# Kernel optimization log

Hardware: AMD Instinct MI355X
Metric: run time of the kernel (lower is better)

The kernel has to match this reference:

```python
import jax, jax.numpy as jnp
import numpy as np
from jax import lax

AGG_HOPS = 3
RANK_K = 10
NEG = -1e9


def _aggregate(embs, agg_w, agg_b, W_last, b_last):
    # GIKT-style multi-hop mean aggregation: embs[j] has shape [B, n1..nj, D]
    embs = list(embs)
    for i in range(AGG_HOPS):
        for j in range(AGG_HOPS - i):
            s = jnp.mean(embs[j + 1], axis=-2) + embs[j]
            embs[j] = jnp.tanh(s @ agg_w[j].T + agg_b[j])
    return jnp.tanh(embs[0] @ W_last.T + b_last)


def _hops(nodes0, tabA, tabB):
    # alternating bipartite neighbor expansion: [B] -> [B,n] -> [B,n,n] -> ...
    lst = [nodes0]
    for i in range(AGG_HOPS):
        tab = tabA if i % 2 == 0 else tabB
        lst.append(tab[lst[-1]])
    return lst


def _forward(user, question, response, mask, q_neighbors, s_neighbors, u_neighbors,
             q_neighbors_2, qs_index, emb_question, emb_question_2, emb_skill,
             emb_user, emb_response, w1_q, w2_q, W_ih, W_hh, b_ih, b_hh,
             agg_w, agg_b, W_agg_last, b_agg_last, W_query, b_query, W_key, b_key,
             W_w, b_w, W_fusion, b_fusion):
    B, T = question.shape
    D = emb_question.shape[1]
    emb_q_all = emb_question[question]  # [B,T,D], used for recap similarity
    wA, wB = W_w[0, :D], W_w[0, D:]     # MLP_W(cat(Q,K)) = Q@wA + K@wB + b

    def predict(qs_concat, states, svalid):
        ql = (qs_concat @ W_query.T + b_query) @ wA          # [B,Lq]
        kl = (states @ W_key.T + b_key) @ wB                 # [B,Ls]
        logit = ql[:, :, None] + kl[:, None, :] + b_w[0]     # [B,Lq,Ls]
        logit = jnp.where(svalid[:, None, :], logit, NEG)
        Lq, Ls = logit.shape[1], logit.shape[2]
        alpha = jax.nn.softmax(logit.reshape(B, -1), axis=1).reshape(B, Lq, Ls)
        g = jnp.einsum('bqd,bsd->bqs', qs_concat, states)
        return jax.nn.sigmoid(jnp.sum(alpha * g, axis=(1, 2)))

    def step(carry, t):
        h, c, sh = carry
        q_t, u_t, r_t = question[:, t], user[:, t], response[:, t]
        m = (mask[:, t] == 1)[:, None]  # [B,1]
        # question-skill GNN branch
        embs_q = [(emb_question if i % 2 == 0 else emb_skill)[n]
                  for i, n in enumerate(_hops(q_t, q_neighbors, s_neighbors))]
        e1 = jnp.where(m, _aggregate(embs_q, agg_w, agg_b, W_agg_last, b_agg_last),
                       emb_question[q_t])
        # user-question GNN branch
        embs_u = [(emb_user if i % 2 == 0 else emb_question_2)[n]
                  for i, n in enumerate(_hops(u_t, u_neighbors, q_neighbors_2))]
        e2 = jnp.where(m, _aggregate(embs_u, agg_w, agg_b, W_agg_last, b_agg_last),
                       emb_question_2[q_t])
        e_hat = w1_q * e1 + w2_q * e2
        e_t = jax.nn.relu(jnp.concatenate([e_hat, emb_response[r_t]], axis=1)
                          @ W_fusion.T + b_fusion)
        # masked LSTMCell (torch gate order i,f,g,o); dropout in eval mode
        gates = e_t @ W_ih.T + b_ih + h @ W_hh.T + b_hh
        gi, gf, gg, go = jnp.split(gates, 4, axis=1)
        c2 = jax.nn.sigmoid(gf) * c + jax.nn.sigmoid(gi) * jnp.tanh(gg)
        h2 = jax.nn.sigmoid(go) * jnp.tanh(c2)
        h = jnp.where(m, h2, h)
        c = jnp.where(m, c2, c)
        sh = lax.dynamic_update_slice(sh, h[:, None, :], (0, t, 0))
        # next question + its related skills
        q_next = question[:, t + 1]
        emb_qn = emb_question[q_next]
        qs_concat = jnp.concatenate([emb_qn[:, None, :], emb_skill[qs_index[q_next]]], axis=1)
        # soft recap: top-k past states by (detached) question similarity
        scores = lax.stop_gradient(jnp.einsum('btd,bd->bt', emb_q_all, emb_qn))
        valid_t = jnp.arange(T) < t
        scores = jnp.where(valid_t[None, :], scores, NEG)
        _, idx = lax.top_k(scores, RANK_K)                    # [B,K]
        sel = jnp.take_along_axis(sh, idx[:, :, None], axis=1)  # [B,K,D]
        svalid = jnp.concatenate([jnp.ones((B, 1), bool), valid_t[idx]], axis=1)
        states = jnp.concatenate([h[:, None, :], sel], axis=1)  # [B,1+K,D]
        y = predict(qs_concat, states, svalid)
        return (h, c, sh), y

    h0 = jnp.zeros((B, D), jnp.float32)
    sh0 = jnp.zeros((B, T, D), jnp.float32)
    _, ys = lax.scan(step, (h0, h0, sh0), jnp.arange(T - 1))
    return jnp.concatenate([jnp.full((B, 1), 0.5, jnp.float32), ys.T], axis=1)


def setup_inputs() -> dict:
    B, T, D = 32, 50, 100
    NQ, NS, NU = 20000, 500, 10000
    NBR, SPQ = 6, 4
    key = jax.random.key(0)
    ks = iter(jax.random.split(key, 48))
    nrm = lambda shape, sc: jax.random.normal(next(ks), shape, jnp.float32) * sc
    ri = lambda shape, hi: jax.random.randint(next(ks), shape, 0, hi, jnp.int32)
    s = 1.0 / float(np.sqrt(D))
    return {
        'user': ri((B, T), NU), 'question': ri((B, T), NQ),
        'response': ri((B, T), 2), 'mask': ri((B, T), 2),
        'q_neighbors': ri((NQ, NBR), NS), 's_neighbors': ri((NS, NBR), NQ),
        'u_neighbors': ri((NU, NBR), NQ), 'q_neighbors_2': ri((NQ, NBR), NU),
        'qs_index': ri((NQ, SPQ), NS),
        'emb_question': nrm((NQ, D), 0.1), 'emb_question_2': nrm((NQ, D), 0.1),
        'emb_skill': nrm((NS, D), 0.1), 'emb_user': nrm((NU, D), 0.1),
        'emb_response': nrm((2, D), 0.1),
        'w1_q': jnp.float32(0.5), 'w2_q': jnp.float32(0.5),
        'W_ih': nrm((4 * D, D), s), 'W_hh': nrm((4 * D, D), s),
        'b_ih': jnp.zeros((4 * D,), jnp.float32), 'b_hh': jnp.zeros((4 * D,), jnp.float32),
        'agg_w': nrm((3, D, D), s), 'agg_b': jnp.zeros((3, D), jnp.float32),
        'W_agg_last': nrm((D, D), s), 'b_agg_last': jnp.zeros((D,), jnp.float32),
        'W_query': nrm((D, D), s), 'b_query': jnp.zeros((D,), jnp.float32),
        'W_key': nrm((D, D), s), 'b_key': jnp.zeros((D,), jnp.float32),
        'W_w': nrm((1, 2 * D), s), 'b_w': jnp.zeros((1,), jnp.float32),
        'W_fusion': nrm((D, 2 * D), s), 'b_fusion': jnp.zeros((D,), jnp.float32),
    }


def reference(user, question, response, mask, q_neighbors, s_neighbors, u_neighbors,
              q_neighbors_2, qs_index, emb_question, emb_question_2, emb_skill,
              emb_user, emb_response, w1_q, w2_q, W_ih, W_hh, b_ih, b_hh,
              agg_w, agg_b, W_agg_last, b_agg_last, W_query, b_query, W_key, b_key,
              W_w, b_w, W_fusion, b_fusion):
    return _forward(user, question, response, mask, q_neighbors, s_neighbors,
                    u_neighbors, q_neighbors_2, qs_index, emb_question,
                    emb_question_2, emb_skill, emb_user, emb_response, w1_q, w2_q,
                    W_ih, W_hh, b_ih, b_hh, agg_w, agg_b, W_agg_last, b_agg_last,
                    W_query, b_query, W_key, b_key, W_w, b_w, W_fusion, b_fusion)
```

## Files before the change

### kernel.cpp

```cpp
#include <hip/hip_runtime.h>
#include <hip/hip_bf16.h>

#define BSZ 32
#define TT 50
#define TS 49
#define PH 101

#define OFF_GPRE  0u
#define OFF_QL    627200u
#define OFF_IDX   639744u
#define OFF_NV    655424u
#define OFF_QSC   656992u
#define OFF_E1    1440992u
#define OFF_E2    1597792u

#define RLF(v,l) __uint_as_float(__builtin_amdgcn_readlane(__float_as_uint(v), (l)))

__device__ __forceinline__ float tanh_fast(float x) {
    float e = __expf(2.f * x);
    return 1.f - __fdividef(2.f, e + 1.f);
}
__device__ __forceinline__ float sigm_fast(float x) {
    return __fdividef(1.f, 1.f + __expf(-x));
}
__device__ __forceinline__ float dot4(float4 a, float4 b) {
    return a.x*b.x + a.y*b.y + a.z*b.z + a.w*b.w;
}
__device__ __forceinline__ float dot100(const float* __restrict__ w, const float* __restrict__ x) {
    float acc = 0.f;
    for (int k = 0; k < 100; k += 4)
        acc += dot4(*(const float4*)(w + k), *(const float4*)(x + k));
    return acc;
}

__global__ __launch_bounds__(384, 5) void kagg(
    const int* __restrict__ user, const int* __restrict__ question, const int* __restrict__ mask,
    const int* __restrict__ qnbr, const int* __restrict__ snbr,
    const int* __restrict__ unbr, const int* __restrict__ qnbr2,
    const float* __restrict__ embQ, const float* __restrict__ embQ2, const float* __restrict__ embS,
    const float* __restrict__ embU,
    const float* __restrict__ aggw, const float* __restrict__ aggb,
    const float* __restrict__ wlast, const float* __restrict__ blast,
    float* __restrict__ WS)
{
    int bid = blockIdx.x;
    int pair = bid >> 1, which = bid & 1;
    int b = pair / TS, t = pair - b*TS;
    int tid = threadIdx.x;
    int mm = mask[b*TT + t];
    float* outE = WS + (which ? OFF_E2 : OFF_E1) + (size_t)pair*100;

    if (mm != 1) {
        int q_t = question[b*TT + t];
        const float* src = which ? embQ2 : embQ;
        if (tid < 100) outE[tid] = src[(size_t)q_t*100 + tid];
        return;
    }

    int root = which ? user[b*TT + t] : question[b*TT + t];
    const int*   tabA = which ? unbr  : qnbr;
    const int*   tabB = which ? qnbr2 : snbr;
    const float* embE = which ? embU  : embQ;
    const float* embO = which ? embQ2 : embS;

    __shared__ __align__(16) float b2in[36*108];
    __shared__ __align__(16) float x1[6*108];
    __shared__ float s2v1b[600];
    __shared__ float v1a[600];
    __shared__ __align__(16) float x0[104], v0a[104], v0b[104];
    __shared__ int n1[8], n2[36], n3[216];

    if (tid < 6) n1[tid] = tabA[root*6 + tid];
    __syncthreads();
    if (tid < 36) n2[tid] = tabB[n1[tid/6]*6 + (tid % 6)];
    __syncthreads();
    if (tid < 216) n3[tid] = tabA[n2[tid/6]*6 + (tid % 6)];
    __syncthreads();
    for (int e = tid; e < 3600; e += 384) {
        int v = e / 100, d = e - v*100;
        float acc = embE[(size_t)n2[v]*100 + d];
        float s3 = 0.f;
        const int* p = n3 + v*6;
        for (int c = 0; c < 6; ++c) s3 += embO[(size_t)p[c]*100 + d];
        b2in[v*108 + d] = acc + s3 * (1.f/6.f);
    }
    for (int e = tid; e < 600; e += 384) {
        int a = e / 100, d = e - a*100;
        float acc = embO[(size_t)n1[a]*100 + d];
        float s = 0.f;
        for (int c = 0; c < 6; ++c) s += embE[(size_t)n2[a*6 + c]*100 + d];
        x1[a*108 + d] = acc + s * (1.f/6.f);
    }
    if (tid < 100) {
        float acc = embE[(size_t)root*100 + tid];
        float s = 0.f;
        for (int a = 0; a < 6; ++a) s += embO[(size_t)n1[a]*100 + tid];
        x0[tid] = acc + s * (1.f/6.f);
    }
    __syncthreads();
    if (tid < 300) {
        int dblk = tid / 6, a = tid - dblk*6, d0 = dblk*2;
        const float* wp = aggw + 20000 + d0*100;
        const float* xb = b2in + a*648;
        float a0[6], a1[6];
        #pragma unroll
        for (int c = 0; c < 6; ++c) { a0[c] = 0.f; a1[c] = 0.f; }
        #pragma unroll
        for (int j = 0; j < 25; ++j) {
            float4 r0 = *(const float4*)(wp + 4*j);
            float4 r1 = *(const float4*)(wp + 100 + 4*j);
            #pragma unroll
            for (int c = 0; c < 6; ++c) {
                float4 x = *(const float4*)(xb + c*108 + 4*j);
                a0[c] += dot4(r0, x);
                a1[c] += dot4(r1, x);
            }
        }
        float bi0 = aggb[200 + d0], bi1 = aggb[200 + d0 + 1];
        float o0 = 0.f, o1 = 0.f;
        #pragma unroll
        for (int c = 0; c < 6; ++c) { o0 += tanh_fast(bi0 + a0[c]); o1 += tanh_fast(bi1 + a1[c]); }
        s2v1b[a*100 + d0] = o0; s2v1b[a*100 + d0 + 1] = o1;
    } else if (tid < 350) {
        int d0 = (tid - 300)*2;
        const float* wp = aggw + 10000 + d0*100;
        float a0[6], a1[6];
        #pragma unroll
        for (int c = 0; c < 6; ++c) { a0[c] = 0.f; a1[c] = 0.f; }
        #pragma unroll
        for (int j = 0; j < 25; ++j) {
            float4 r0 = *(const float4*)(wp + 4*j);
            float4 r1 = *(const float4*)(wp + 100 + 4*j);
            #pragma unroll
            for (int c = 0; c < 6; ++c) {
                float4 x = *(const float4*)(x1 + c*108 + 4*j);
                a0[c] += dot4(r0, x);
                a1[c] += dot4(r1, x);
            }
        }
        #pragma unroll
        for (int c = 0; c < 6; ++c) {
            v1a[c*100 + d0]     = tanh_fast(aggb[100 + d0] + a0[c]);
            v1a[c*100 + d0 + 1] = tanh_fast(aggb[100 + d0 + 1] + a1[c]);
        }
    } else if (tid < 375) {
        int d0 = (tid - 350)*4;
        const float* wp = aggw + d0*100;
        float a0 = 0.f, a1 = 0.f, a2 = 0.f, a3 = 0.f;
        #pragma unroll
        for (int j = 0; j < 25; ++j) {
            float4 x = *(const float4*)(x0 + 4*j);
            a0 += dot4(*(const float4*)(wp + 4*j), x);
            a1 += dot4(*(const float4*)(wp + 100 + 4*j), x);
            a2 += dot4(*(const float4*)(wp + 200 + 4*j), x);
            a3 += dot4(*(const float4*)(wp + 300 + 4*j), x);
        }
        v0a[d0]   = tanh_fast(aggb[d0] + a0);
        v0a[d0+1] = tanh_fast(aggb[d0+1] + a1);
        v0a[d0+2] = tanh_fast(aggb[d0+2] + a2);
        v0a[d0+3] = tanh_fast(aggb[d0+3] + a3);
    }
    __syncthreads();
    for (int e = tid; e < 600; e += 384) {
        int a = e / 100, d = e - a*100;
        x1[a*108 + d] = v1a[a*100 + d] + s2v1b[a*100 + d]*(1.f/6.f);
    }
    if (tid < 100) {
        float s = 0.f;
        for (int a = 0; a < 6; ++a) s += v1a[a*100 + tid];
        x0[tid] = v0a[tid] + s*(1.f/6.f);
    }
    __syncthreads();
    if (tid < 50) {
        int d0 = tid*2;
        const float* wp = aggw + 10000 + d0*100;
        float a0[6], a1[6];
        #pragma unroll
        for (int c = 0; c < 6; ++c) { a0[c] = 0.f; a1[c] = 0.f; }
        #pragma unroll
        for (int j = 0; j < 25; ++j) {
            float4 r0 = *(const float4*)(wp + 4*j);
            float4 r1 = *(const float4*)(wp + 100 + 4*j);
            #pragma unroll
            for (int c = 0; c < 6; ++c) {
                float4 x = *(const float4*)(x1 + c*108 + 4*j);
                a0[c] += dot4(r0, x);
                a1[c] += dot4(r1, x);
            }
        }
        #pragma unroll
        for (int c = 0; c < 6; ++c) {
            s2v1b[c*100 + d0]     = tanh_fast(aggb[100 + d0] + a0[c]);
            s2v1b[c*100 + d0 + 1] = tanh_fast(aggb[100 + d0 + 1] + a1[c]);
        }
    } else if (tid >= 64 && tid < 89) {
        int d0 = (tid - 64)*4;
        const float* wp = aggw + d0*100;
        float a0 = 0.f, a1 = 0.f, a2 = 0.f, a3 = 0.f;
        #pragma unroll
        for (int j = 0; j < 25; ++j) {
            float4 x = *(const float4*)(x0 + 4*j);
            a0 += dot4(*(const float4*)(wp + 4*j), x);
            a1 += dot4(*(const float4*)(wp + 100 + 4*j), x);
            a2 += dot4(*(const float4*)(wp + 200 + 4*j), x);
            a3 += dot4(*(const float4*)(wp + 300 + 4*j), x);
        }
        v0b[d0]   = tanh_fast(aggb[d0] + a0);
        v0b[d0+1] = tanh_fast(aggb[d0+1] + a1);
        v0b[d0+2] = tanh_fast(aggb[d0+2] + a2);
        v0b[d0+3] = tanh_fast(aggb[d0+3] + a3);
    }
    __syncthreads();
    if (tid < 100) {
        float s = 0.f;
        for (int a = 0; a < 6; ++a) s += s2v1b[a*100 + tid];
        x0[tid] = v0b[tid] + s*(1.f/6.f);
    }
    __syncthreads();
    if (tid < 25) {
        int d0 = tid*4;
        const float* wp = aggw + d0*100;
        float a0 = 0.f, a1 = 0.f, a2 = 0.f, a3 = 0.f;
        #pragma unroll
        for (int j = 0; j < 25; ++j) {
            float4 x = *(const float4*)(x0 + 4*j);
            a0 += dot4(*(const float4*)(wp + 4*j), x);
            a1 += dot4(*(const float4*)(wp + 100 + 4*j), x);
            a2 += dot4(*(const float4*)(wp + 200 + 4*j), x);
            a3 += dot4(*(const float4*)(wp + 300 + 4*j), x);
        }
        v0a[d0]   = tanh_fast(aggb[d0] + a0);
        v0a[d0+1] = tanh_fast(aggb[d0+1] + a1);
        v0a[d0+2] = tanh_fast(aggb[d0+2] + a2);
        v0a[d0+3] = tanh_fast(aggb[d0+3] + a3);
    }
    __syncthreads();
    if (tid < 25) {
        int d0 = tid*4;
        const float* wp = wlast + d0*100;
        float a0 = 0.f, a1 = 0.f, a2 = 0.f, a3 = 0.f;
        #pragma unroll
        for (int j = 0; j < 25; ++j) {
            float4 x = *(const float4*)(v0a + 4*j);
            a0 += dot4(*(const float4*)(wp + 4*j), x);
            a1 += dot4(*(const float4*)(wp + 100 + 4*j), x);
            a2 += dot4(*(const float4*)(wp + 200 + 4*j), x);
            a3 += dot4(*(const float4*)(wp + 300 + 4*j), x);
        }
        outE[d0]   = tanh_fast(blast[d0] + a0);
        outE[d0+1] = tanh_fast(blast[d0+1] + a1);
        outE[d0+2] = tanh_fast(blast[d0+2] + a2);
        outE[d0+3] = tanh_fast(blast[d0+3] + a3);
    }
}

__global__ __launch_bounds__(256) void kfuse(
    const int* __restrict__ question, const int* __restrict__ response,
    const int* __restrict__ qsidx,
    const float* __restrict__ embQ, const float* __restrict__ embS, const float* __restrict__ embR,
    const float* __restrict__ w1p, const float* __restrict__ w2p,
    const float* __restrict__ wfus, const float* __restrict__ bfus,
    const float* __restrict__ wih, const float* __restrict__ bih, const float* __restrict__ bhh,
    const float* __restrict__ wq, const float* __restrict__ bq, const float* __restrict__ ww,
    float* __restrict__ WS)
{
    int bid = blockIdx.x;
    int b = bid / TS, t = bid - b*TS;
    int tid = threadIdx.x;
    size_t bt = (size_t)b*TS + t;

    __shared__ __align__(16) float sEIN[200], sET[104], sEQN[104], sVQ[104];
    __shared__ float sWW[200], sQSCm[500], sScore[56], sCq[1];

    int r_t = response[b*TT + t];
    int qn  = question[b*TT + t + 1];
    float w1 = w1p[0], w2 = w2p[0];
    if (tid < 100)
        sEIN[tid] = w1*WS[OFF_E1 + bt*100 + tid] + w2*WS[OFF_E2 + bt*100 + tid];
    else if (tid < 200)
        sEIN[tid] = embR[r_t*100 + (tid - 100)];
    else
        for (int i = tid - 200; i < 200; i += 56) sWW[i] = ww[i];
    __syncthreads();
    if (tid < 100) {
        float acc = bfus[tid];
        const float* wr = wfus + tid*200;
        for (int k = 0; k < 200; k += 4)
            acc += dot4(*(const float4*)(wr + k), *(const float4*)(sEIN + k));
        sET[tid] = fmaxf(acc, 0.f);
    } else if (tid < 200) {
        int k = tid - 100;
        float acc = 0.f;
        for (int d = 0; d < 100; ++d) acc += sWW[d]*wq[d*100 + k];
        sVQ[k] = acc;
    } else if (tid == 200) {
        float acc = 0.f;
        for (int d = 0; d < 100; ++d) acc += bq[d]*sWW[d];
        sCq[0] = acc;
    } else if (tid >= 201 && tid < 251) {
        int d = tid - 201;
        sEQN[d]      = embQ[(size_t)qn*100 + d];
        sEQN[d + 50] = embQ[(size_t)qn*100 + d + 50];
    }
    __syncthreads();
    if (tid < 200) {
        for (int i = tid; i < 500; i += 200) {
            int q = i / 100, d = i - q*100;
            float val = (q == 0) ? sEQN[d] : embS[(size_t)qsidx[qn*4 + (q-1)]*100 + d];
            sQSCm[i] = val;
            WS[OFF_QSC + bt*500 + i] = val;
        }
    } else if (tid < 250) {
        int tp = tid - 200;
        if (tp < t) {
            int qq = question[b*TT + tp];
            const float* er = embQ + (size_t)qq*100;
            float acc = 0.f;
            for (int k = 0; k < 100; k += 4)
                acc += dot4(*(const float4*)(er + k), *(const float4*)(sEQN + k));
            sScore[tp] = acc;
        }
    }
    __syncthreads();
    for (int o = tid; o < 400; o += 256)
        WS[OFF_GPRE + bt*400 + o] = bih[o] + bhh[o] + dot100(wih + o*100, sET);
    if (tid < 80) {
        int q = tid >> 4, k0 = tid & 15;
        float acc = 0.f;
        #pragma unroll
        for (int j = 0; j < 7; ++j) {
            int k = k0 + 16*j;
            if (k < 100) acc = fmaf(sQSCm[q*100 + k], sVQ[k], acc);
        }
        acc += __shfl_xor(acc, 1); acc += __shfl_xor(acc, 2);
        acc += __shfl_xor(acc, 4); acc += __shfl_xor(acc, 8);
        if (k0 == 0) WS[OFF_QL + bt*8 + q] = acc + sCq[0];
    }
    if (tid == 255) {
        int nv = t < 10 ? t : 10;
        ((int*)(WS + OFF_NV))[bt] = nv;
        int* idxp = (int*)(WS + OFF_IDX) + bt*10;
        unsigned long long taken = 0ull;
        for (int p = 0; p < 10; ++p) {
            int bi = 0;
            if (p < nv) {
                float best = -3.0e38f;
                for (int tp2 = 0; tp2 < t; ++tp2) {
                    if (!((taken >> tp2) & 1ull) && sScore[tp2] > best) { best = sScore[tp2]; bi = tp2; }
                }
                taken |= (1ull << bi);
            }
            idxp[p] = bi;
        }
    }
}

__global__ __launch_bounds__(576) void kseq(
    const int* __restrict__ mask, const float* __restrict__ whh,
    const float* __restrict__ wk, const float* __restrict__ bk,
    const float* __restrict__ ww, const float* __restrict__ bwp,
    const float* __restrict__ WS, float* __restrict__ out)
{
    int b = blockIdx.x, tid = threadIdx.x, lane = tid & 63;
    __shared__ float sQSCall[TS*500];
    __shared__ float sSH[TS*PH + 3];
    __shared__ float sQLall[TS*8];
    __shared__ int   sIdxAll[TS*10];
    __shared__ int   sNvAll[TS];
    __shared__ int   sMask[TT];
    __shared__ float sH[104], sC[104], sG[400], sVKl[104];
    __shared__ float sKL2[2][12], sGv2[2][64];
    __shared__ float sCkBw[2];

    size_t b0 = (size_t)b*TS;
    int g = tid - 64;
    bool isGate = (g >= 0 && g < 400);

    float4 wv[25];
    if (isGate) {
        #pragma unroll
        for (int j = 0; j < 25; ++j) wv[j] = *(const float4*)(whh + g*100 + 4*j);
    }
    float gpre = isGate ? WS[OFF_GPRE + b0*400 + g] : 0.f;

    for (int i = tid; i < TS*500; i += 576) sQSCall[i] = WS[OFF_QSC + b0*500 + i];
    for (int i = tid; i < TS*8;   i += 576) sQLall[i]  = WS[OFF_QL + b0*8 + i];
    for (int i = tid; i < TS*10;  i += 576) sIdxAll[i] = ((const int*)(WS + OFF_IDX))[b0*10 + i];
    for (int i = tid; i < TS;     i += 576) sNvAll[i]  = ((const int*)(WS + OFF_NV))[b0 + i];
    if (tid < TT) sMask[tid] = mask[b*TT + tid];
    if (tid < 104) { sH[tid] = 0.f; sC[tid] = 0.f; }
    if (tid >= 104 && tid < 204) {
        int k = tid - 104;
        float acc = 0.f;
        for (int d = 0; d < 100; ++d) acc += ww[100 + d]*wk[d*100 + k];
        sVKl[k] = acc;
    }
    if (tid == 204) {
        float acc = 0.f;
        for (int d = 0; d < 100; ++d) acc += bk[d]*ww[100 + d];
        sCkBw[0] = acc; sCkBw[1] = bwp[0];
    }
    if (tid == 205) out[b*TT] = 0.5f;
    __syncthreads();
    float ck = sCkBw[0], bw = sCkBw[1];

    for (int t = 0; t < TS; ++t) {
        int par = t & 1;
        if (isGate) {
            float hA = sH[lane];
            float hB = sH[64 + (lane % 36)];
            float gpre_nx = 0.f;
            if (t + 1 < TS) gpre_nx = WS[OFF_GPRE + (b0 + t + 1)*400 + g];
            float a0 = 0.f, a1 = 0.f, a2 = 0.f, a3 = 0.f;
            #pragma unroll
            for (int j = 0; j < 25; ++j) {
                const int kb = 4*j;
                float h0, h1, h2, h3;
                if (kb < 64) {
                    h0 = RLF(hA, kb);   h1 = RLF(hA, kb+1);
                    h2 = RLF(hA, kb+2); h3 = RLF(hA, kb+3);
                } else {
                    h0 = RLF(hB, kb-64); h1 = RLF(hB, kb-63);
                    h2 = RLF(hB, kb-62); h3 = RLF(hB, kb-61);
                }
                a0 = fmaf(h0, wv[j].x, a0);
                a1 = fmaf(h1, wv[j].y, a1);
                a2 = fmaf(h2, wv[j].z, a2);
                a3 = fmaf(h3, wv[j].w, a3);
            }
            sG[g] = (a0 + a1) + (a2 + a3) + gpre;
            gpre = gpre_nx;
        } else if (tid >= 512) {
            int nv = sNvAll[t];
            if (lane < 60) {
                bool isKL = lane < 10;
                int s = isKL ? (lane + 1) : (((lane - 10) % 10) + 1);
                int q = isKL ? 0 : ((lane - 10) / 10);
                if (s <= nv) {
                    const float* st = sSH + sIdxAll[t*10 + s - 1]*PH;
                    const float* xp = isKL ? sVKl : (sQSCall + t*500 + q*100);
                    float c0 = 0.f, c1 = 0.f, c2 = 0.f, c3 = 0.f;
                    #pragma unroll
                    for (int k = 0; k < 100; k += 4) {
                        c0 = fmaf(st[k],   xp[k],   c0);
                        c1 = fmaf(st[k+1], xp[k+1], c1);
                        c2 = fmaf(st[k+2], xp[k+2], c2);
                        c3 = fmaf(st[k+3], xp[k+3], c3);
                    }
                    float acc = (c0 + c1) + (c2 + c3);
                    if (isKL) sKL2[par][s] = acc + ck;
                    else      sGv2[par][q*12 + s] = acc;
                }
            }
        } else if (tid < 64 && t > 0) {
            int tau = t - 1, par2 = tau & 1;
            int nv = sNvAll[tau];
            int dd = lane >> 3, k0 = lane & 7;
            if (dd < 6) {
                const float* xp = (dd == 0) ? sVKl : (sQSCall + tau*500 + (dd-1)*100);
                float acc = 0.f;
                #pragma unroll
                for (int jj = 0; jj < 13; ++jj) {
                    int k = k0 + 8*jj;
                    if (k < 100) acc = fmaf(sH[k], xp[k], acc);
                }
                acc += __shfl_xor(acc, 1); acc += __shfl_xor(acc, 2); acc += __shfl_xor(acc, 4);
                if (k0 == 0) {
                    if (dd == 0) sKL2[par2][0] = acc + ck;
                    else         sGv2[par2][(dd-1)*12] = acc;
                }
            }
            int q = lane / 11, s = lane - q*11;
            bool valid = (lane < 55) && (s <= nv);
            float lg = valid ? (sQLall[tau*8 + q] + sKL2[par2][s] + bw) : 0.f;
            float e  = valid ? __expf(lg) : 0.f;
            float gv = valid ? sGv2[par2][q*12 + s] : 0.f;
            float se = e, sg = e*gv;
            #pragma unroll
            for (int m = 1; m < 64; m <<= 1) { se += __shfl_xor(se, m); sg += __shfl_xor(sg, m); }
            if (lane == 0) out[b*TT + tau + 1] = __fdividef(1.f, 1.f + __expf(-__fdividef(sg, se)));
        }
        __syncthreads();
        if (g >= 0 && g < 100) {
            float gi = sG[g], gf = sG[100+g], gg = sG[200+g], go = sG[300+g];
            float c2 = sigm_fast(gf)*sC[g] + sigm_fast(gi)*tanh_fast(gg);
            float h2 = sigm_fast(go)*tanh_fast(c2);
            if (sMask[t] == 1) { sH[g] = h2; sC[g] = c2; }
            sSH[t*PH + g] = sH[g];
        }
        __syncthreads();
    }
    if (tid < 64) {
        int tau = TS - 1, par2 = tau & 1;
        int nv = sNvAll[tau];
        int dd = lane >> 3, k0 = lane & 7;
        if (dd < 6) {
            const float* xp = (dd == 0) ? sVKl : (sQSCall + tau*500 + (dd-1)*100);
            float acc = 0.f;
            #pragma unroll
            for (int jj = 0; jj < 13; ++jj) {
                int k = k0 + 8*jj;
                if (k < 100) acc = fmaf(sH[k], xp[k], acc);
            }
            acc += __shfl_xor(acc, 1); acc += __shfl_xor(acc, 2); acc += __shfl_xor(acc, 4);
            if (k0 == 0) {
                if (dd == 0) sKL2[par2][0] = acc + ck;
                else         sGv2[par2][(dd-1)*12] = acc;
            }
        }
        int q = lane / 11, s = lane - q*11;
        bool valid = (lane < 55) && (s <= nv);
        float lg = valid ? (sQLall[tau*8 + q] + sKL2[par2][s] + bw) : 0.f;
        float e  = valid ? __expf(lg) : 0.f;
        float gv = valid ? sGv2[par2][q*12 + s] : 0.f;
        float se = e, sg = e*gv;
        #pragma unroll
        for (int m = 1; m < 64; m <<= 1) { se += __shfl_xor(se, m); sg += __shfl_xor(sg, m); }
        if (lane == 0) out[b*TT + tau + 1] = __fdividef(1.f, 1.f + __expf(-__fdividef(sg, se)));
    }
}

extern "C" void kernel_launch(void* const* d_in, const int* in_sizes, int n_in,
                              void* d_out, int out_size, void* d_ws, size_t ws_size,
                              hipStream_t stream) {
    const int* user      = (const int*)d_in[0];
    const int* question  = (const int*)d_in[1];
    const int* response  = (const int*)d_in[2];
    const int* mask      = (const int*)d_in[3];
    const int* qnbr      = (const int*)d_in[4];
    const int* snbr      = (const int*)d_in[5];
    const int* unbr      = (const int*)d_in[6];
    const int* qnbr2     = (const int*)d_in[7];
    const int* qsidx     = (const int*)d_in[8];
    const float* embQ    = (const float*)d_in[9];
    const float* embQ2   = (const float*)d_in[10];
    const float* embS    = (const float*)d_in[11];
    const float* embU    = (const float*)d_in[12];
    const float* embR    = (const float*)d_in[13];
    const float* w1      = (const float*)d_in[14];
    const float* w2      = (const float*)d_in[15];
    const float* wih     = (const float*)d_in[16];
    const float* whh     = (const float*)d_in[17];
    const float* bih     = (const float*)d_in[18];
    const float* bhh     = (const float*)d_in[19];
    const float* aggw    = (const float*)d_in[20];
    const float* aggb    = (const float*)d_in[21];
    const float* wlast   = (const float*)d_in[22];
    const float* blast   = (const float*)d_in[23];
    const float* wq      = (const float*)d_in[24];
    const float* bq      = (const float*)d_in[25];
    const float* wk      = (const float*)d_in[26];
    const float* bk      = (const float*)d_in[27];
    const float* ww      = (const float*)d_in[28];
    const float* bwp     = (const float*)d_in[29];
    const float* wfus    = (const float*)d_in[30];
    const float* bfus    = (const float*)d_in[31];
    float* WS = (float*)d_ws;
    float* out = (float*)d_out;

    hipLaunchKernelGGL(kagg, dim3(2*BSZ*TS), dim3(384), 0, stream,
                       user, question, mask, qnbr, snbr, unbr, qnbr2,
                       embQ, embQ2, embS, embU, aggw, aggb, wlast, blast, WS);
    hipLaunchKernelGGL(kfuse, dim3(BSZ*TS), dim3(256), 0, stream,
                       question, response, qsidx, embQ, embS, embR,
                       w1, w2, wfus, bfus, wih, bih, bhh, wq, bq, ww, WS);
    hipLaunchKernelGGL(kseq, dim3(BSZ), dim3(576), 0, stream,
                       mask, whh, wk, bk, ww, bwp, WS, out);
}
```

Baseline: 438.4 us.

## Hoist weight-vector precompute, vectorize gathers, parallelize fuse matvecs and top-k

The constant query/key projection vectors (W_w folded into W_query/W_key and their biases) are now computed once by an extra block in the aggregation kernel, instead of once per (b,t) block in kfuse and once per batch in kseq. The aggregation kernel shrinks to 256 threads, uses float4 gathers of the embedding rows and gives each thread 4 output rows in the hop-2 matvec. kfuse now computes its fusion and gate-input matvecs with 16-lane cooperative dot products and shuffle reductions. Its serial single-thread top-10 selection becomes a wave-wide argmax reduction. These changes add a cross-kernel dependency on the workspace constants and rely on the extra block finishing before kfuse reads them.

```diff
diff --git a/kernel.cpp b/kernel.cpp
--- a/kernel.cpp
+++ b/kernel.cpp
@@ -6,13 +6,16 @@
 #define TS 49
 #define PH 101
 
-#define OFF_GPRE  0u
-#define OFF_QL    627200u
-#define OFF_IDX   639744u
-#define OFF_NV    655424u
-#define OFF_QSC   656992u
-#define OFF_E1    1440992u
-#define OFF_E2    1597792u
+#define OFF_VQ    0u
+#define OFF_VK    128u
+#define OFF_SC    256u
+#define OFF_GPRE  288u
+#define OFF_QL    627488u
+#define OFF_IDX   640032u
+#define OFF_NV    655712u
+#define OFF_QSC   657280u
+#define OFF_E1    1441280u
+#define OFF_E2    1598080u
 
 #define RLF(v,l) __uint_as_float(__builtin_amdgcn_readlane(__float_as_uint(v), (l)))
 
@@ -26,14 +29,8 @@
 __device__ __forceinline__ float dot4(float4 a, float4 b) {
     return a.x*b.x + a.y*b.y + a.z*b.z + a.w*b.w;
 }
-__device__ __forceinline__ float dot100(const float* __restrict__ w, const float* __restrict__ x) {
-    float acc = 0.f;
-    for (int k = 0; k < 100; k += 4)
-        acc += dot4(*(const float4*)(w + k), *(const float4*)(x + k));
-    return acc;
-}
-
-__global__ __launch_bounds__(384, 5) void kagg(
+
+__global__ __launch_bounds__(256, 5) void kagg(
     const int* __restrict__ user, const int* __restrict__ question, const int* __restrict__ mask,
     const int* __restrict__ qnbr, const int* __restrict__ snbr,
     const int* __restrict__ unbr, const int* __restrict__ qnbr2,
@@ -41,19 +38,47 @@
     const float* __restrict__ embU,
     const float* __restrict__ aggw, const float* __restrict__ aggb,
     const float* __restrict__ wlast, const float* __restrict__ blast,
+    const float* __restrict__ wq, const float* __restrict__ bq,
+    const float* __restrict__ wk, const float* __restrict__ bk,
+    const float* __restrict__ ww, const float* __restrict__ bwp,
     float* __restrict__ WS)
 {
     int bid = blockIdx.x;
+    int tid = threadIdx.x;
+
+    if (bid == 2*BSZ*TS) {
+        if (tid < 100) {
+            float a = 0.f;
+            for (int d = 0; d < 100; ++d) a += ww[d] * wq[d*100 + tid];
+            WS[OFF_VQ + tid] = a;
+        } else if (tid < 200) {
+            int k = tid - 100;
+            float a = 0.f;
+            for (int d = 0; d < 100; ++d) a += ww[100 + d] * wk[d*100 + k];
+            WS[OFF_VK + k] = a;
+        } else if (tid == 200) {
+            float a = 0.f;
+            for (int d = 0; d < 100; ++d) a += bq[d] * ww[d];
+            WS[OFF_SC + 0] = a;
+        } else if (tid == 201) {
+            float a = 0.f;
+            for (int d = 0; d < 100; ++d) a += bk[d] * ww[100 + d];
+            WS[OFF_SC + 1] = a;
+        } else if (tid == 202) {
+            WS[OFF_SC + 2] = bwp[0];
+        }
+        return;
+    }
+
     int pair = bid >> 1, which = bid & 1;
     int b = pair / TS, t = pair - b*TS;
-    int tid = threadIdx.x;
     int mm = mask[b*TT + t];
     float* outE = WS + (which ? OFF_E2 : OFF_E1) + (size_t)pair*100;
 
     if (mm != 1) {
         int q_t = question[b*TT + t];
-        const float* src = which ? embQ2 : embQ;
-        if (tid < 100) outE[tid] = src[(size_t)q_t*100 + tid];
+        const float4* src = (const float4*)((which ? embQ2 : embQ) + (size_t)q_t*100);
+        if (tid < 25) ((float4*)outE)[tid] = src[tid];
         return;
     }
 
@@ -62,6 +87,8 @@
     const int*   tabB = which ? qnbr2 : snbr;
     const float* embE = which ? embU  : embQ;
     const float* embO = which ? embQ2 : embS;
+    const float4* eE = (const float4*)embE;
+    const float4* eO = (const float4*)embO;
 
     __shared__ __align__(16) float b2in[36*108];
     __shared__ __align__(16) float x1[6*108];
@@ -76,53 +103,81 @@
     __syncthreads();
     if (tid < 216) n3[tid] = tabA[n2[tid/6]*6 + (tid % 6)];
     __syncthreads();
-    for (int e = tid; e < 3600; e += 384) {
-        int v = e / 100, d = e - v*100;
-        float acc = embE[(size_t)n2[v]*100 + d];
-        float s3 = 0.f;
+    for (int i4 = tid; i4 < 900; i4 += 256) {
+        int v = i4 / 25, j = i4 - v*25;
+        float4 a = eE[(size_t)n2[v]*25 + j];
+        float4 s = make_float4(0.f, 0.f, 0.f, 0.f);
         const int* p = n3 + v*6;
-        for (int c = 0; c < 6; ++c) s3 += embO[(size_t)p[c]*100 + d];
-        b2in[v*108 + d] = acc + s3 * (1.f/6.f);
-    }
-    for (int e = tid; e < 600; e += 384) {
-        int a = e / 100, d = e - a*100;
-        float acc = embO[(size_t)n1[a]*100 + d];
-        float s = 0.f;
-        for (int c = 0; c < 6; ++c) s += embE[(size_t)n2[a*6 + c]*100 + d];
-        x1[a*108 + d] = acc + s * (1.f/6.f);
-    }
-    if (tid < 100) {
-        float acc = embE[(size_t)root*100 + tid];
-        float s = 0.f;
-        for (int a = 0; a < 6; ++a) s += embO[(size_t)n1[a]*100 + tid];
-        x0[tid] = acc + s * (1.f/6.f);
-    }
-    __syncthreads();
-    if (tid < 300) {
-        int dblk = tid / 6, a = tid - dblk*6, d0 = dblk*2;
+        #pragma unroll
+        for (int c = 0; c < 6; ++c) {
+            float4 o = eO[(size_t)p[c]*25 + j];
+            s.x += o.x; s.y += o.y; s.z += o.z; s.w += o.w;
+        }
+        float4 r = make_float4(a.x + s.x*(1.f/6.f), a.y + s.y*(1.f/6.f),
+                               a.z + s.z*(1.f/6.f), a.w + s.w*(1.f/6.f));
+        *(float4*)(b2in + v*108 + 4*j) = r;
+    }
+    for (int i4 = tid; i4 < 150; i4 += 256) {
+        int a = i4 / 25, j = i4 - a*25;
+        float4 base = eO[(size_t)n1[a]*25 + j];
+        float4 s = make_float4(0.f, 0.f, 0.f, 0.f);
+        #pragma unroll
+        for (int c = 0; c < 6; ++c) {
+            float4 o = eE[(size_t)n2[a*6 + c]*25 + j];
+            s.x += o.x; s.y += o.y; s.z += o.z; s.w += o.w;
+        }
+        float4 r = make_float4(base.x + s.x*(1.f/6.f), base.y + s.y*(1.f/6.f),
+                               base.z + s.z*(1.f/6.f), base.w + s.w*(1.f/6.f));
+        *(float4*)(x1 + a*108 + 4*j) = r;
+    }
+    if (tid >= 160 && tid < 185) {
+        int j = tid - 160;
+        float4 base = eE[(size_t)root*25 + j];
+        float4 s = make_float4(0.f, 0.f, 0.f, 0.f);
+        #pragma unroll
+        for (int a = 0; a < 6; ++a) {
+            float4 o = eO[(size_t)n1[a]*25 + j];
+            s.x += o.x; s.y += o.y; s.z += o.z; s.w += o.w;
+        }
+        float4 r = make_float4(base.x + s.x*(1.f/6.f), base.y + s.y*(1.f/6.f),
+                               base.z + s.z*(1.f/6.f), base.w + s.w*(1.f/6.f));
+        *(float4*)(x0 + 4*j) = r;
+    }
+    __syncthreads();
+    if (tid < 150) {
+        int dblk = tid / 6, a = tid - dblk*6, d0 = dblk*4;
         const float* wp = aggw + 20000 + d0*100;
         const float* xb = b2in + a*648;
-        float a0[6], a1[6];
-        #pragma unroll
-        for (int c = 0; c < 6; ++c) { a0[c] = 0.f; a1[c] = 0.f; }
+        float acc[4][6];
+        #pragma unroll
+        for (int r = 0; r < 4; ++r)
+            #pragma unroll
+            for (int c = 0; c < 6; ++c) acc[r][c] = 0.f;
         #pragma unroll
         for (int j = 0; j < 25; ++j) {
             float4 r0 = *(const float4*)(wp + 4*j);
             float4 r1 = *(const float4*)(wp + 100 + 4*j);
+            float4 r2 = *(const float4*)(wp + 200 + 4*j);
+            float4 r3 = *(const float4*)(wp + 300 + 4*j);
             #pragma unroll
             for (int c = 0; c < 6; ++c) {
                 float4 x = *(const float4*)(xb + c*108 + 4*j);
-                a0[c] += dot4(r0, x);
-                a1[c] += dot4(r1, x);
-            }
-        }
-        float bi0 = aggb[200 + d0], bi1 = aggb[200 + d0 + 1];
-        float o0 = 0.f, o1 = 0.f;
-        #pragma unroll
-        for (int c = 0; c < 6; ++c) { o0 += tanh_fast(bi0 + a0[c]); o1 += tanh_fast(bi1 + a1[c]); }
-        s2v1b[a*100 + d0] = o0; s2v1b[a*100 + d0 + 1] = o1;
-    } else if (tid < 350) {
-        int d0 = (tid - 300)*2;
+                acc[0][c] += dot4(r0, x);
+                acc[1][c] += dot4(r1, x);
+                acc[2][c] += dot4(r2, x);
+                acc[3][c] += dot4(r3, x);
+            }
+        }
+        #pragma unroll
+        for (int r = 0; r < 4; ++r) {
+            float bia = aggb[200 + d0 + r];
+            float o = 0.f;
+            #pragma unroll
+            for (int c = 0; c < 6; ++c) o += tanh_fast(bia + acc[r][c]);
+            s2v1b[a*100 + d0 + r] = o;
+        }
+    } else if (tid >= 160 && tid < 210) {
+        int d0 = (tid - 160)*2;
         const float* wp = aggw + 10000 + d0*100;
         float a0[6], a1[6];
         #pragma unroll
@@ -143,8 +198,8 @@
             v1a[c*100 + d0]     = tanh_fast(aggb[100 + d0] + a0[c]);
             v1a[c*100 + d0 + 1] = tanh_fast(aggb[100 + d0 + 1] + a1[c]);
         }
-    } else if (tid < 375) {
-        int d0 = (tid - 350)*4;
+    } else if (tid >= 216 && tid < 241) {
+        int d0 = (tid - 216)*4;
         const float* wp = aggw + d0*100;
         float a0 = 0.f, a1 = 0.f, a2 = 0.f, a3 = 0.f;
         #pragma unroll
@@ -161,14 +216,16 @@
         v0a[d0+3] = tanh_fast(aggb[d0+3] + a3);
     }
     __syncthreads();
-    for (int e = tid; e < 600; e += 384) {
+    for (int e = tid; e < 600; e += 256) {
         int a = e / 100, d = e - a*100;
         x1[a*108 + d] = v1a[a*100 + d] + s2v1b[a*100 + d]*(1.f/6.f);
     }
-    if (tid < 100) {
+    if (tid >= 128 && tid < 228) {
+        int d = tid - 128;
         float s = 0.f;
-        for (int a = 0; a < 6; ++a) s += v1a[a*100 + tid];
-        x0[tid] = v0a[tid] + s*(1.f/6.f);
+        #pragma unroll
+        for (int a = 0; a < 6; ++a) s += v1a[a*100 + d];
+        x0[d] = v0a[d] + s*(1.f/6.f);
     }
     __syncthreads();
     if (tid < 50) {
@@ -213,6 +270,7 @@
     __syncthreads();
     if (tid < 100) {
         float s = 0.f;
+        #pragma unroll
         for (int a = 0; a < 6; ++a) s += s2v1b[a*100 + tid];
         x0[tid] = v0b[tid] + s*(1.f/6.f);
     }
@@ -247,21 +305,19 @@
             a2 += dot4(*(const float4*)(wp + 200 + 4*j), x);
             a3 += dot4(*(const float4*)(wp + 300 + 4*j), x);
         }
-        outE[d0]   = tanh_fast(blast[d0] + a0);
-        outE[d0+1] = tanh_fast(blast[d0+1] + a1);
-        outE[d0+2] = tanh_fast(blast[d0+2] + a2);
-        outE[d0+3] = tanh_fast(blast[d0+3] + a3);
+        float4 r = make_float4(tanh_fast(blast[d0] + a0), tanh_fast(blast[d0+1] + a1),
+                               tanh_fast(blast[d0+2] + a2), tanh_fast(blast[d0+3] + a3));
+        *(float4*)(outE + d0) = r;
     }
 }
 
-__global__ __launch_bounds__(256) void kfuse(
+__global__ __launch_bounds__(256, 6) void kfuse(
     const int* __restrict__ question, const int* __restrict__ response,
     const int* __restrict__ qsidx,
     const float* __restrict__ embQ, const float* __restrict__ embS, const float* __restrict__ embR,
     const float* __restrict__ w1p, const float* __restrict__ w2p,
     const float* __restrict__ wfus, const float* __restrict__ bfus,
     const float* __restrict__ wih, const float* __restrict__ bih, const float* __restrict__ bhh,
-    const float* __restrict__ wq, const float* __restrict__ bq, const float* __restrict__ ww,
     float* __restrict__ WS)
 {
     int bid = blockIdx.x;
@@ -269,96 +325,113 @@
     int tid = threadIdx.x;
     size_t bt = (size_t)b*TS + t;
 
-    __shared__ __align__(16) float sEIN[200], sET[104], sEQN[104], sVQ[104];
-    __shared__ float sWW[200], sQSCm[500], sScore[56], sCq[1];
+    __shared__ __align__(16) float sEIN[200], sET[112], sEQN[104], sQSCm[500];
+    __shared__ float sScore[52];
 
     int r_t = response[b*TT + t];
     int qn  = question[b*TT + t + 1];
-    float w1 = w1p[0], w2 = w2p[0];
-    if (tid < 100)
-        sEIN[tid] = w1*WS[OFF_E1 + bt*100 + tid] + w2*WS[OFF_E2 + bt*100 + tid];
-    else if (tid < 200)
+    if (tid < 100) {
+        sEIN[tid] = w1p[0]*WS[OFF_E1 + bt*100 + tid] + w2p[0]*WS[OFF_E2 + bt*100 + tid];
+    } else if (tid < 200) {
         sEIN[tid] = embR[r_t*100 + (tid - 100)];
-    else
-        for (int i = tid - 200; i < 200; i += 56) sWW[i] = ww[i];
-    __syncthreads();
-    if (tid < 100) {
-        float acc = bfus[tid];
-        const float* wr = wfus + tid*200;
-        for (int k = 0; k < 200; k += 4)
-            acc += dot4(*(const float4*)(wr + k), *(const float4*)(sEIN + k));
-        sET[tid] = fmaxf(acc, 0.f);
-    } else if (tid < 200) {
-        int k = tid - 100;
-        float acc = 0.f;
-        for (int d = 0; d < 100; ++d) acc += sWW[d]*wq[d*100 + k];
-        sVQ[k] = acc;
-    } else if (tid == 200) {
-        float acc = 0.f;
-        for (int d = 0; d < 100; ++d) acc += bq[d]*sWW[d];
-        sCq[0] = acc;
-    } else if (tid >= 201 && tid < 251) {
-        int d = tid - 201;
+    } else if (tid < 250) {
+        int d = tid - 200;
         sEQN[d]      = embQ[(size_t)qn*100 + d];
         sEQN[d + 50] = embQ[(size_t)qn*100 + d + 50];
     }
     __syncthreads();
-    if (tid < 200) {
-        for (int i = tid; i < 500; i += 200) {
-            int q = i / 100, d = i - q*100;
-            float val = (q == 0) ? sEQN[d] : embS[(size_t)qsidx[qn*4 + (q-1)]*100 + d];
-            sQSCm[i] = val;
-            WS[OFF_QSC + bt*500 + i] = val;
-        }
-    } else if (tid < 250) {
-        int tp = tid - 200;
+    int slot = tid >> 4, k0 = tid & 15;
+    #pragma unroll
+    for (int rp = 0; rp < 7; ++rp) {
+        int row = rp*16 + slot;
+        float acc = 0.f;
+        if (row < 100) {
+            const float* wr = wfus + row*200;
+            #pragma unroll
+            for (int m = 0; m < 4; ++m) {
+                int f4i = k0 + 16*m;
+                if (f4i < 50)
+                    acc += dot4(*(const float4*)(wr + 4*f4i), *(const float4*)(sEIN + 4*f4i));
+            }
+        }
+        acc += __shfl_xor(acc, 1); acc += __shfl_xor(acc, 2);
+        acc += __shfl_xor(acc, 4); acc += __shfl_xor(acc, 8);
+        if (row < 100 && k0 == 0) sET[row] = fmaxf(acc + bfus[row], 0.f);
+    }
+    __syncthreads();
+    #pragma unroll 4
+    for (int rp = 0; rp < 25; ++rp) {
+        int row = rp*16 + slot;
+        const float* wr = wih + row*100;
+        float acc = 0.f;
+        #pragma unroll
+        for (int m = 0; m < 2; ++m) {
+            int f4i = k0 + 16*m;
+            if (f4i < 25)
+                acc += dot4(*(const float4*)(wr + 4*f4i), *(const float4*)(sET + 4*f4i));
+        }
+        acc += __shfl_xor(acc, 1); acc += __shfl_xor(acc, 2);
+        acc += __shfl_xor(acc, 4); acc += __shfl_xor(acc, 8);
+        if (k0 == 0) WS[OFF_GPRE + bt*400 + row] = acc + bih[row] + bhh[row];
+    }
+    if (tid < 125) {
+        int q = tid / 25, j = tid - q*25;
+        float4 val = (q == 0) ? *(const float4*)(sEQN + 4*j)
+                              : ((const float4*)embS)[(size_t)qsidx[qn*4 + (q-1)]*25 + j];
+        *(float4*)(sQSCm + q*100 + 4*j) = val;
+        *(float4*)(WS + OFF_QSC + bt*500 + q*100 + 4*j) = val;
+    } else if (tid >= 128 && tid < 128 + TS) {
+        int tp = tid - 128;
         if (tp < t) {
             int qq = question[b*TT + tp];
             const float* er = embQ + (size_t)qq*100;
             float acc = 0.f;
-            for (int k = 0; k < 100; k += 4)
-                acc += dot4(*(const float4*)(er + k), *(const float4*)(sEQN + k));
+            #pragma unroll
+            for (int k = 0; k < 25; ++k)
+                acc += dot4(*(const float4*)(er + 4*k), *(const float4*)(sEQN + 4*k));
             sScore[tp] = acc;
         }
     }
     __syncthreads();
-    for (int o = tid; o < 400; o += 256)
-        WS[OFF_GPRE + bt*400 + o] = bih[o] + bhh[o] + dot100(wih + o*100, sET);
     if (tid < 80) {
-        int q = tid >> 4, k0 = tid & 15;
+        int q = tid >> 4, kk = tid & 15;
         float acc = 0.f;
         #pragma unroll
         for (int j = 0; j < 7; ++j) {
-            int k = k0 + 16*j;
-            if (k < 100) acc = fmaf(sQSCm[q*100 + k], sVQ[k], acc);
+            int k = kk + 16*j;
+            if (k < 100) acc = fmaf(sQSCm[q*100 + k], WS[OFF_VQ + k], acc);
         }
         acc += __shfl_xor(acc, 1); acc += __shfl_xor(acc, 2);
         acc += __shfl_xor(acc, 4); acc += __shfl_xor(acc, 8);
-        if (k0 == 0) WS[OFF_QL + bt*8 + q] = acc + sCq[0];
-    }
-    if (tid == 255) {
+        if (kk == 0) WS[OFF_QL + bt*8 + q] = acc + WS[OFF_SC + 0];
+    }
+    if (tid >= 128 && tid < 192) {
+        int lane = tid - 128;
         int nv = t < 10 ? t : 10;
-        ((int*)(WS + OFF_NV))[bt] = nv;
         int* idxp = (int*)(WS + OFF_IDX) + bt*10;
-        unsigned long long taken = 0ull;
+        if (lane == 0) ((int*)(WS + OFF_NV))[bt] = nv;
+        float v = (lane < t) ? sScore[lane] : -3.0e38f;
+        int myidx = lane;
+        int taken = 0;
         for (int p = 0; p < 10; ++p) {
-            int bi = 0;
+            float vv = taken ? -3.0e38f : v;
+            int ii = myidx;
+            #pragma unroll
+            for (int m = 1; m < 64; m <<= 1) {
+                float v2 = __shfl_xor(vv, m);
+                int   i2 = __shfl_xor(ii, m);
+                if (v2 > vv || (v2 == vv && i2 < ii)) { vv = v2; ii = i2; }
+            }
             if (p < nv) {
-                float best = -3.0e38f;
-                for (int tp2 = 0; tp2 < t; ++tp2) {
-                    if (!((taken >> tp2) & 1ull) && sScore[tp2] > best) { best = sScore[tp2]; bi = tp2; }
-                }
-                taken |= (1ull << bi);
-            }
-            idxp[p] = bi;
+                if (lane == 0) idxp[p] = ii;
+                if (myidx == ii) taken = 1;
+            } else if (lane == 0) idxp[p] = 0;
         }
     }
 }
 
 __global__ __launch_bounds__(576) void kseq(
     const int* __restrict__ mask, const float* __restrict__ whh,
-    const float* __restrict__ wk, const float* __restrict__ bk,
-    const float* __restrict__ ww, const float* __restrict__ bwp,
     const float* __restrict__ WS, float* __restrict__ out)
 {
     int b = blockIdx.x, tid = threadIdx.x, lane = tid & 63;
@@ -370,7 +443,6 @@
     __shared__ int   sMask[TT];
     __shared__ float sH[104], sC[104], sG[400], sVKl[104];
     __shared__ float sKL2[2][12], sGv2[2][64];
-    __shared__ float sCkBw[2];
 
     size_t b0 = (size_t)b*TS;
     int g = tid - 64;
@@ -389,20 +461,10 @@
     for (int i = tid; i < TS;     i += 576) sNvAll[i]  = ((const int*)(WS + OFF_NV))[b0 + i];
     if (tid < TT) sMask[tid] = mask[b*TT + tid];
     if (tid < 104) { sH[tid] = 0.f; sC[tid] = 0.f; }
-    if (tid >= 104 && tid < 204) {
-        int k = tid - 104;
-        float acc = 0.f;
-        for (int d = 0; d < 100; ++d) acc += ww[100 + d]*wk[d*100 + k];
-        sVKl[k] = acc;
-    }
-    if (tid == 204) {
-        float acc = 0.f;
-        for (int d = 0; d < 100; ++d) acc += bk[d]*ww[100 + d];
-        sCkBw[0] = acc; sCkBw[1] = bwp[0];
-    }
-    if (tid == 205) out[b*TT] = 0.5f;
-    __syncthreads();
-    float ck = sCkBw[0], bw = sCkBw[1];
+    if (tid >= 104 && tid < 204) sVKl[tid - 104] = WS[OFF_VK + (tid - 104)];
+    if (tid == 204) out[b*TT] = 0.5f;
+    float ck = WS[OFF_SC + 1], bw = WS[OFF_SC + 2];
+    __syncthreads();
 
     for (int t = 0; t < TS; ++t) {
         int par = t & 1;
@@ -558,12 +620,13 @@
     float* WS = (float*)d_ws;
     float* out = (float*)d_out;
 
-    hipLaunchKernelGGL(kagg, dim3(2*BSZ*TS), dim3(384), 0, stream,
+    hipLaunchKernelGGL(kagg, dim3(2*BSZ*TS + 1), dim3(256), 0, stream,
                        user, question, mask, qnbr, snbr, unbr, qnbr2,
-                       embQ, embQ2, embS, embU, aggw, aggb, wlast, blast, WS);
+                       embQ, embQ2, embS, embU, aggw, aggb, wlast, blast,
+                       wq, bq, wk, bk, ww, bwp, WS);
     hipLaunchKernelGGL(kfuse, dim3(BSZ*TS), dim3(256), 0, stream,
                        question, response, qsidx, embQ, embS, embR,
-                       w1, w2, wfus, bfus, wih, bih, bhh, wq, bq, ww, WS);
+                       w1, w2, wfus, bfus, wih, bih, bhh, WS);
     hipLaunchKernelGGL(kseq, dim3(BSZ), dim3(576), 0, stream,
-                       mask, whh, wk, bk, ww, bwp, WS, out);
+                       mask, whh, WS, out);
 }
```

After: 472.1 us. 7.7% more time.
